# Kernel optimization log

Measured on AMD Instinct MI355X. Metric: run time of the kernel, lower is better.

Reference implementation:

```python
import jax, jax.numpy as jnp
import numpy as np

A = 200.0          # penalty increment
NUM_STRUCT = 4     # classes 0..3: abutment, girder, deck, parapet
# (i, j, mult): weight[i]+=mult*A and weight[j]+=mult*A when GT says center_z_i < center_z_j
# but prediction says center_z_i >= center_z_j (and both classes present in GT and Pr).
PAIRS = [(0, 1, 1.0), (1, 2, 1.0), (2, 3, 1.0), (0, 2, 2.0), (1, 3, 2.0), (0, 3, 3.0)]


def setup_inputs() -> dict:
    key = jax.random.key(0)
    k1, k2, k3, k4, k5 = jax.random.split(key, 5)
    B, N, C = 16, 65536, 5
    pred = jax.random.normal(k1, (B, N, C), dtype=jnp.float32)
    target = jax.random.randint(k2, (B, N), 0, C, dtype=jnp.int32)
    points = jax.random.normal(k3, (B, N, 9), dtype=jnp.float32)
    pred_previous = jax.random.normal(k4, (B * N, C), dtype=jnp.float32)
    target_previous = jax.random.randint(k5, (B * N,), 0, C, dtype=jnp.int64)
    return {"pred": pred, "target": target, "points": points,
            "pred_previous": pred_previous, "target_previous": target_previous}


def _batch_weights(pred, target, points):
    """Per-batch class weights [B, C] following the original branch logic."""
    B, N, C = pred.shape
    z = points[:, :, 2]                                    # [B, N]
    pred_label = jnp.argmax(pred, axis=-1)                 # [B, N]
    cls = jnp.arange(NUM_STRUCT)
    gt_oh = (target[..., None] == cls).astype(z.dtype)     # [B, N, 4]
    pr_oh = (pred_label[..., None] == cls).astype(z.dtype)
    gt_cnt = gt_oh.sum(axis=1)                             # [B, 4]
    pr_cnt = pr_oh.sum(axis=1)
    gt_mean = jnp.einsum('bn,bnc->bc', z, gt_oh) / jnp.maximum(gt_cnt, 1.0)
    pr_mean = jnp.einsum('bn,bnc->bc', z, pr_oh) / jnp.maximum(pr_cnt, 1.0)
    GT = gt_cnt > 0
    PR = pr_cnt > 0

    w = jnp.ones((B, C), dtype=z.dtype)
    # class predicted but absent in GT
    miss = jnp.logical_and(jnp.logical_not(GT), PR).astype(z.dtype)  # [B, 4]
    w = w.at[:, :NUM_STRUCT].add(A * miss)
    # vertical-order violations
    for i, j, m in PAIRS:
        cond = (GT[:, i] & PR[:, i] & GT[:, j] & PR[:, j]
                & (gt_mean[:, i] < gt_mean[:, j])
                & (pr_mean[:, i] >= pr_mean[:, j]))
        add = (m * A) * cond.astype(z.dtype)
        w = w.at[:, i].add(add).at[:, j].add(add)
    return w


def reference(pred, target, points, pred_previous, target_previous):
    B, N, C = pred.shape
    w = _batch_weights(pred, target, points)               # [B, C]
    # weighted cross-entropy over pred_previous, computed once via per-class sums
    logp = jax.nn.log_softmax(pred_previous, axis=-1)      # [M, C]
    nll = -jnp.take_along_axis(logp, target_previous[:, None], axis=1)[:, 0]  # [M]
    s = jax.ops.segment_sum(nll, target_previous, num_segments=C)             # [C]
    n = jax.ops.segment_sum(jnp.ones_like(nll), target_previous, num_segments=C)
    # torch mean-reduction weighted CE: sum_n w[t_n]*nll_n / sum_n w[t_n]
    loss_b = (w @ s) / (w @ n)                             # [B]
    return loss_b.sum()
```

## Files before the change

kernel.cpp:

```cpp
#include <hip/hip_runtime.h>
#include <math.h>

#define A_W 200.0f
#define B_BATCH 16
#define N_PTS 65536
#define C_CLS 5
#define BN (B_BATCH * N_PTS)

#define STAT_BLOCKS 1024
#define NLL_BLOCKS 1024
#define TPB 256
#define NLL_BASE 16384


__device__ inline float wave_reduce_f(float v) {
#pragma unroll
    for (int off = 32; off > 0; off >>= 1)
        v += __shfl_down(v, off, 64);
    return v;
}

__global__ __launch_bounds__(TPB)
void main_kernel(const float* __restrict__ pred,
                 const int* __restrict__ target,
                 const float* __restrict__ points,
                 const float* __restrict__ prev,
                 const unsigned* __restrict__ tprev_u32,
                 float* __restrict__ ws) {
    __shared__ float sm[16];
    __shared__ int sflag;
    const int bid = blockIdx.x;
    const int tid = threadIdx.x;
    const int lane = tid & 63;
    const int wv = tid >> 6;

    if (tid < 16) sm[tid] = 0.0f;

    if (bid >= STAT_BLOCKS && wv == 0) {
        unsigned w = tprev_u32[2 * lane + 1];
        unsigned long long bal = __ballot(w != 0u);
        if (tid == 0) sflag = (bal != 0ull) ? 1 : 0;
    }
    __syncthreads();

    if (bid < STAT_BLOCKS) {
        const int b = bid >> 6;
        const int chunk = bid & 63;
        const size_t n0 = (size_t)b * N_PTS + (size_t)chunk * 1024 + (size_t)tid * 4;

        const float4* __restrict__ p4 = (const float4*)(pred + n0 * 5);
        float4 q0 = p4[0], q1 = p4[1], q2 = p4[2], q3 = p4[3], q4 = p4[4];
        const int4 tg = *(const int4*)(target + n0);
        const float* __restrict__ pb = points + n0 * 9;
        float zv[4] = {pb[2], pb[11], pb[20], pb[29]};

        float xs[4][5] = {
            {q0.x, q0.y, q0.z, q0.w, q1.x},
            {q1.y, q1.z, q1.w, q2.x, q2.y},
            {q2.z, q2.w, q3.x, q3.y, q3.z},
            {q3.w, q4.x, q4.y, q4.z, q4.w}};
        int tgt[4] = {tg.x, tg.y, tg.z, tg.w};

        float gc0 = 0, gc1 = 0, gc2 = 0, gc3 = 0;
        float pc0 = 0, pc1 = 0, pc2 = 0, pc3 = 0;
        float gz0 = 0, gz1 = 0, gz2 = 0, gz3 = 0;
        float pz0 = 0, pz1 = 0, pz2 = 0, pz3 = 0;

#pragma unroll
        for (int j = 0; j < 4; ++j) {
            float x0 = xs[j][0], x1 = xs[j][1], x2 = xs[j][2],
                  x3 = xs[j][3], x4 = xs[j][4];
            int am = 0;
            float bv = x0;
            if (x1 > bv) { bv = x1; am = 1; }
            if (x2 > bv) { bv = x2; am = 2; }
            if (x3 > bv) { bv = x3; am = 3; }
            if (x4 > bv) { bv = x4; am = 4; }
            float z = zv[j];
            int t = tgt[j];
            if (t == 0) { gc0 += 1.f; gz0 += z; }
            else if (t == 1) { gc1 += 1.f; gz1 += z; }
            else if (t == 2) { gc2 += 1.f; gz2 += z; }
            else if (t == 3) { gc3 += 1.f; gz3 += z; }
            if (am == 0) { pc0 += 1.f; pz0 += z; }
            else if (am == 1) { pc1 += 1.f; pz1 += z; }
            else if (am == 2) { pc2 += 1.f; pz2 += z; }
            else if (am == 3) { pc3 += 1.f; pz3 += z; }
        }

        float vals[16] = {gc0, gc1, gc2, gc3, pc0, pc1, pc2, pc3,
                          gz0, gz1, gz2, gz3, pz0, pz1, pz2, pz3};
#pragma unroll
        for (int k = 0; k < 16; ++k) {
            float r = wave_reduce_f(vals[k]);
            if (lane == 0) atomicAdd(&sm[k], r);
        }
        __syncthreads();
        if (tid < 16) ws[(size_t)bid * 16 + tid] = sm[tid];
    } else {
        const int nb = bid - STAT_BLOCKS;
        const size_t k0 = (size_t)nb * 1024 + (size_t)tid * 4;
        const int is32 = sflag;

        const float4* __restrict__ p4 = (const float4*)(prev + k0 * 5);
        float4 q0 = p4[0], q1 = p4[1], q2 = p4[2], q3 = p4[3], q4 = p4[4];

        int tgt[4];
        if (is32) {
            int4 tt = *(const int4*)((const int*)tprev_u32 + k0);
            tgt[0] = tt.x; tgt[1] = tt.y; tgt[2] = tt.z; tgt[3] = tt.w;
        } else {
            int4 a = *(const int4*)((const int*)tprev_u32 + 2 * k0);
            int4 c = *(const int4*)((const int*)tprev_u32 + 2 * k0 + 4);
            tgt[0] = a.x; tgt[1] = a.z; tgt[2] = c.x; tgt[3] = c.z;
        }

        float xs[4][5] = {
            {q0.x, q0.y, q0.z, q0.w, q1.x},
            {q1.y, q1.z, q1.w, q2.x, q2.y},
            {q2.z, q2.w, q3.x, q3.y, q3.z},
            {q3.w, q4.x, q4.y, q4.z, q4.w}};

        float s0 = 0, s1 = 0, s2 = 0, s3 = 0, s4 = 0;
        float c0 = 0, c1 = 0, c2 = 0, c3 = 0, c4 = 0;

#pragma unroll
        for (int j = 0; j < 4; ++j) {
            float x0 = xs[j][0], x1 = xs[j][1], x2 = xs[j][2],
                  x3 = xs[j][3], x4 = xs[j][4];
            float m = fmaxf(fmaxf(fmaxf(x0, x1), fmaxf(x2, x3)), x4);
            float e = __expf(x0 - m) + __expf(x1 - m) + __expf(x2 - m) +
                      __expf(x3 - m) + __expf(x4 - m);
            float lse = m + __logf(e);
            int t = tgt[j];
            float xt = x0;
            xt = (t == 1) ? x1 : xt;
            xt = (t == 2) ? x2 : xt;
            xt = (t == 3) ? x3 : xt;
            xt = (t == 4) ? x4 : xt;
            float nll = lse - xt;
            if (t == 0) { s0 += nll; c0 += 1.f; }
            else if (t == 1) { s1 += nll; c1 += 1.f; }
            else if (t == 2) { s2 += nll; c2 += 1.f; }
            else if (t == 3) { s3 += nll; c3 += 1.f; }
            else { s4 += nll; c4 += 1.f; }
        }

        float vals[10] = {s0, s1, s2, s3, s4, c0, c1, c2, c3, c4};
#pragma unroll
        for (int k = 0; k < 10; ++k) {
            float r = wave_reduce_f(vals[k]);
            if (lane == 0) atomicAdd(&sm[k], r);
        }
        __syncthreads();
        if (tid < 10) ws[NLL_BASE + (size_t)tid * 1024 + nb] = sm[tid];
    }
}

__global__ __launch_bounds__(1024)
void final_kernel(const float* __restrict__ ws, float* __restrict__ out) {
    __shared__ float stat[256];
    __shared__ float sn[10];
    const int t = threadIdx.x;
    const int lane = t & 63;
    const int wv = t >> 6;

    if (t < 256) {
        const int b = t >> 4, v = t & 15;
        const float* p = ws + (size_t)(b * 64) * 16 + v;
        float s = 0.0f;
#pragma unroll 8
        for (int i = 0; i < 64; ++i) s += p[(size_t)i * 16];
        stat[t] = s;
    }
    if (wv >= 4 && wv < 14) {
        const int v = wv - 4;
        const float* p = ws + NLL_BASE + (size_t)v * 1024;
        float s = 0.0f;
#pragma unroll
        for (int k = 0; k < 16; ++k) s += p[lane + 64 * k];
        s = wave_reduce_f(s);
        if (lane == 0) sn[v] = s;
    }
    __syncthreads();

    float loss = 0.0f;
    if (t < B_BATCH) {
        const float* st = stat + t * 16;
        float gc[4], pc[4], gm[4], pm[4];
        bool GT[4], PR[4];
        float w[5] = {1.f, 1.f, 1.f, 1.f, 1.f};
#pragma unroll
        for (int c = 0; c < 4; ++c) {
            gc[c] = st[c];
            pc[c] = st[4 + c];
            GT[c] = gc[c] > 0.0f;
            PR[c] = pc[c] > 0.0f;
            gm[c] = st[8 + c] / fmaxf(gc[c], 1.0f);
            pm[c] = st[12 + c] / fmaxf(pc[c], 1.0f);
            if (!GT[c] && PR[c]) w[c] += A_W;
        }
#define PAIR(i, j, mlt)                                                        \
        {                                                                      \
            bool cond = GT[i] && PR[i] && GT[j] && PR[j] &&                    \
                        (gm[i] < gm[j]) && (pm[i] >= pm[j]);                   \
            float add = (mlt) * A_W * (cond ? 1.0f : 0.0f);                    \
            w[i] += add;                                                       \
            w[j] += add;                                                       \
        }
        PAIR(0, 1, 1.0f)
        PAIR(1, 2, 1.0f)
        PAIR(2, 3, 1.0f)
        PAIR(0, 2, 2.0f)
        PAIR(1, 3, 2.0f)
        PAIR(0, 3, 3.0f)
#undef PAIR
        float num = 0.0f, den = 0.0f;
#pragma unroll
        for (int c = 0; c < C_CLS; ++c) {
            num += w[c] * sn[c];
            den += w[c] * sn[5 + c];
        }
        loss = num / den;
    }
    if (wv == 0) {
#pragma unroll
        for (int off = 8; off > 0; off >>= 1)
            loss += __shfl_down(loss, off, 64);
        if (t == 0) out[0] = loss;
    }
}

extern "C" void kernel_launch(void* const* d_in, const int* in_sizes, int n_in,
                              void* d_out, int out_size, void* d_ws, size_t ws_size,
                              hipStream_t stream) {
    const float* pred = (const float*)d_in[0];
    const int* target = (const int*)d_in[1];
    const float* points = (const float*)d_in[2];
    const float* prev = (const float*)d_in[3];
    const unsigned* tprev = (const unsigned*)d_in[4];
    float* ws = (float*)d_ws;
    float* out = (float*)d_out;

    hipLaunchKernelGGL(main_kernel, dim3(STAT_BLOCKS + NLL_BLOCKS), dim3(TPB),
                       0, stream, pred, target, points, prev, tprev, ws);
    hipLaunchKernelGGL(final_kernel, dim3(1), dim3(1024), 0, stream, ws, out);
}
```

Baseline: 116.4 us.

## Fuse final reduction into main kernel via last-block atomic counter

Removes the separate single-block final kernel. Blocks now atomically accumulate their partial statistics into small per-batch and striped NLL accumulators in the workspace, and the last block to finish, detected through an atomic ticket counter, computes the weights and the loss. The workspace is zeroed with a memset before the launch. This trades one kernel launch and the serial final pass for global atomics, a memset, and float atomic ordering nondeterminism.

```diff
diff --git a/kernel.cpp b/kernel.cpp
--- a/kernel.cpp
+++ b/kernel.cpp
@@ -5,13 +5,15 @@
 #define B_BATCH 16
 #define N_PTS 65536
 #define C_CLS 5
-#define BN (B_BATCH * N_PTS)
 
 #define STAT_BLOCKS 1024
 #define NLL_BLOCKS 1024
 #define TPB 256
-#define NLL_BASE 16384
-
+#define GRID_BLOCKS (STAT_BLOCKS + NLL_BLOCKS)
+
+#define ACC_NLL 256
+#define ACC_CNT 576
+#define ACC_BYTES ((ACC_CNT + 1) * 4)
 
 __device__ inline float wave_reduce_f(float v) {
 #pragma unroll
@@ -26,9 +28,12 @@
                  const float* __restrict__ points,
                  const float* __restrict__ prev,
                  const unsigned* __restrict__ tprev_u32,
-                 float* __restrict__ ws) {
+                 float* __restrict__ ws,
+                 float* __restrict__ out) {
     __shared__ float sm[16];
+    __shared__ float fsn[10];
     __shared__ int sflag;
+    __shared__ int slast;
     const int bid = blockIdx.x;
     const int tid = threadIdx.x;
     const int lane = tid & 63;
@@ -96,7 +101,7 @@
             if (lane == 0) atomicAdd(&sm[k], r);
         }
         __syncthreads();
-        if (tid < 16) ws[(size_t)bid * 16 + tid] = sm[tid];
+        if (tid < 16) atomicAdd(&ws[b * 16 + tid], sm[tid]);
     } else {
         const int nb = bid - STAT_BLOCKS;
         const size_t k0 = (size_t)nb * 1024 + (size_t)tid * 4;
@@ -153,51 +158,41 @@
             if (lane == 0) atomicAdd(&sm[k], r);
         }
         __syncthreads();
-        if (tid < 10) ws[NLL_BASE + (size_t)tid * 1024 + nb] = sm[tid];
-    }
-}
-
-__global__ __launch_bounds__(1024)
-void final_kernel(const float* __restrict__ ws, float* __restrict__ out) {
-    __shared__ float stat[256];
-    __shared__ float sn[10];
-    const int t = threadIdx.x;
-    const int lane = t & 63;
-    const int wv = t >> 6;
-
-    if (t < 256) {
-        const int b = t >> 4, v = t & 15;
-        const float* p = ws + (size_t)(b * 64) * 16 + v;
+        if (tid < 10) atomicAdd(&ws[ACC_NLL + tid * 32 + (nb & 31)], sm[tid]);
+    }
+
+    __syncthreads();
+    if (tid == 0) {
+        __threadfence();
+        int old = atomicAdd((int*)&ws[ACC_CNT], 1);
+        slast = (old == GRID_BLOCKS - 1) ? 1 : 0;
+    }
+    __syncthreads();
+    if (!slast) return;
+
+    volatile const float* acc = ws;
+
+    if (tid < 10) {
         float s = 0.0f;
-#pragma unroll 8
-        for (int i = 0; i < 64; ++i) s += p[(size_t)i * 16];
-        stat[t] = s;
-    }
-    if (wv >= 4 && wv < 14) {
-        const int v = wv - 4;
-        const float* p = ws + NLL_BASE + (size_t)v * 1024;
-        float s = 0.0f;
-#pragma unroll
-        for (int k = 0; k < 16; ++k) s += p[lane + 64 * k];
-        s = wave_reduce_f(s);
-        if (lane == 0) sn[v] = s;
+#pragma unroll
+        for (int k = 0; k < 32; ++k) s += acc[ACC_NLL + tid * 32 + k];
+        fsn[tid] = s;
     }
     __syncthreads();
 
     float loss = 0.0f;
-    if (t < B_BATCH) {
-        const float* st = stat + t * 16;
+    if (tid < B_BATCH) {
         float gc[4], pc[4], gm[4], pm[4];
         bool GT[4], PR[4];
         float w[5] = {1.f, 1.f, 1.f, 1.f, 1.f};
 #pragma unroll
         for (int c = 0; c < 4; ++c) {
-            gc[c] = st[c];
-            pc[c] = st[4 + c];
+            gc[c] = acc[tid * 16 + c];
+            pc[c] = acc[tid * 16 + 4 + c];
             GT[c] = gc[c] > 0.0f;
             PR[c] = pc[c] > 0.0f;
-            gm[c] = st[8 + c] / fmaxf(gc[c], 1.0f);
-            pm[c] = st[12 + c] / fmaxf(pc[c], 1.0f);
+            gm[c] = acc[tid * 16 + 8 + c] / fmaxf(gc[c], 1.0f);
+            pm[c] = acc[tid * 16 + 12 + c] / fmaxf(pc[c], 1.0f);
             if (!GT[c] && PR[c]) w[c] += A_W;
         }
 #define PAIR(i, j, mlt)                                                        \
@@ -218,8 +213,8 @@
         float num = 0.0f, den = 0.0f;
 #pragma unroll
         for (int c = 0; c < C_CLS; ++c) {
-            num += w[c] * sn[c];
-            den += w[c] * sn[5 + c];
+            num += w[c] * fsn[c];
+            den += w[c] * fsn[5 + c];
         }
         loss = num / den;
     }
@@ -227,7 +222,7 @@
 #pragma unroll
         for (int off = 8; off > 0; off >>= 1)
             loss += __shfl_down(loss, off, 64);
-        if (t == 0) out[0] = loss;
+        if (tid == 0) out[0] = loss;
     }
 }
 
@@ -242,7 +237,7 @@
     float* ws = (float*)d_ws;
     float* out = (float*)d_out;
 
-    hipLaunchKernelGGL(main_kernel, dim3(STAT_BLOCKS + NLL_BLOCKS), dim3(TPB),
-                       0, stream, pred, target, points, prev, tprev, ws);
-    hipLaunchKernelGGL(final_kernel, dim3(1), dim3(1024), 0, stream, ws, out);
+    hipMemsetAsync(ws, 0, ACC_BYTES, stream);
+    hipLaunchKernelGGL(main_kernel, dim3(GRID_BLOCKS), dim3(TPB),
+                       0, stream, pred, target, points, prev, tprev, ws, out);
 }
```

New measurement: 187.8 us. 61.4% more time.
